# Kernel tuning notes

Hardware: AMD Instinct MI355X
Metric: run time of the kernel (lower is better)

The kernel has to match this reference:

```python
import jax, jax.numpy as jnp
import numpy as np

# Kronecker-sparse patterns (a,b,c,d), rightmost factor first, matching KSLinear.
PATTERNS = ((1, 64, 64, 64), (64, 64, 64, 1))
IN_SIZE = PATTERNS[0][0] * PATTERNS[0][2] * PATTERNS[0][3]   # 4096
OUT_SIZE = PATTERNS[-1][0] * PATTERNS[-1][1] * PATTERNS[-1][3]  # 4096
N_TOKENS = 16384


def setup_inputs() -> dict:
    key = jax.random.key(0)
    kx, k0, k1, kb = jax.random.split(key, 4)
    x = jax.random.normal(kx, (N_TOKENS, IN_SIZE), dtype=jnp.float32)
    # factors stored in native 4D (a,b,c,d) layout, uniform(-1/sqrt(c), 1/sqrt(c))
    a, b, c, d = PATTERNS[0]
    s0 = 1.0 / np.sqrt(c)
    f0 = jax.random.uniform(k0, (a, b, c, d), jnp.float32, -s0, s0)
    a, b, c, d = PATTERNS[1]
    s1 = 1.0 / np.sqrt(c)
    f1 = jax.random.uniform(k1, (a, b, c, d), jnp.float32, -s1, s1)
    bound = 1.0 / np.sqrt(IN_SIZE)
    bias = jax.random.uniform(kb, (OUT_SIZE,), jnp.float32, -bound, bound)
    return {"x": x, "f0": f0, "f1": f1, "bias": bias}


def _ks_apply(x, factor, pattern):
    # Apply one Kronecker-sparse factor with support I_a (x) 1_{b,c} (x) I_d.
    a, b, c, d = pattern
    batch = x.shape[:-1]
    x = x.reshape(*batch, a, c, d)                      # (..., a, c, d)
    y = jnp.einsum('...acd,abcd->...abd', x, factor)    # contract over c
    return y.reshape(*batch, a * b * d)


def reference(x, f0, f1, bias):
    y = _ks_apply(x, f0, PATTERNS[0])
    y = _ks_apply(y, f1, PATTERNS[1])
    return y + bias
```

## Files before the change

### kernel.cpp

```cpp
#include <hip/hip_runtime.h>
#include <cstdint>
#include <cstddef>

#define DI __device__ __forceinline__

using f32x4  = __attribute__((ext_vector_type(4))) float;
using bf16x8 = __attribute__((ext_vector_type(8))) short;
using u32x2  = __attribute__((ext_vector_type(2))) unsigned int;
using u32x4  = __attribute__((ext_vector_type(4))) unsigned int;

constexpr int NT = 16384;
constexpr int NF = 4096;

DI unsigned short f2bf(float f) {
  union { float f; unsigned u; } v; v.f = f;
  unsigned u = v.u;
  u += 0x7fffu + ((u >> 16) & 1u);
  return (unsigned short)(u >> 16);
}

DI void gload_lds16(const void* g, void* l) {
  __builtin_amdgcn_global_load_lds(
      (const __attribute__((address_space(1))) unsigned int*)g,
      (__attribute__((address_space(3))) unsigned int*)l, 16, 0, 0);
}

DI void bar_lgkm() {
  asm volatile("s_waitcnt lgkmcnt(0)" ::: "memory");
  __builtin_amdgcn_s_barrier();
  __builtin_amdgcn_sched_barrier(0);
}
#define BAR_VM(N)                                              \
  do {                                                         \
    asm volatile("s_waitcnt vmcnt(" #N ")" ::: "memory");      \
    __builtin_amdgcn_s_barrier();                              \
    __builtin_amdgcn_sched_barrier(0);                         \
  } while (0)

__global__ void ks_prep(const float* __restrict__ f0, const float* __restrict__ f1,
                        unsigned short* __restrict__ f0s, unsigned short* __restrict__ f1s) {
  int tid = blockIdx.x * 256 + threadIdx.x;
  if (tid < 262144) {
    int d = tid & 63, c = (tid >> 6) & 63, b = tid >> 12;
    f0s[d * 4096 + b * 64 + c] = f2bf(f0[tid]);
  } else {
    int t2 = tid - 262144;
    f1s[t2] = f2bf(f1[t2]);
  }
}

__global__ __launch_bounds__(512, 4) void ks1(
    const float* __restrict__ x, const unsigned short* __restrict__ f0s,
    unsigned short* __restrict__ yp)
{
  __shared__ __align__(16) char L[32768 + 2 * 16640];
  char* const Xb0 = L;
  char* const Xb1 = L + 16384;
  char* const Yb0 = L + 32768;
  char* const Yb1 = L + 32768 + 16640;

  const int w  = blockIdx.x;
  const int tt = (w & 7) | ((w >> 6) << 3);
  const int dg = (w >> 3) & 7;
  const long T0 = (long)tt * 128;

  const int tid = threadIdx.x, lane = tid & 63, wv = tid >> 6;
  const int l15 = lane & 15, lq = lane >> 4;
  const int d = dg * 8 + wv;

  bf16x8 fA[4][2];
  #pragma unroll
  for (int bt = 0; bt < 4; ++bt)
    #pragma unroll
    for (int kh = 0; kh < 2; ++kh)
      fA[bt][kh] = *(const bf16x8*)(f0s + (size_t)d * 4096 + (bt * 16 + l15) * 64 + kh * 32 + lq * 8);

  const int st_t = tid >> 5, st_c0 = (tid >> 1) & 15, st_dq = tid & 1;
  const float* const xrow0 = x + (T0 + st_t) * (long)NF + dg * 8 + st_dq * 4;
  const int wkey = (st_t & 7) << 4;

  f32x4 r0, r1, r2, r3;
  auto issue = [&](int st) {
    const float* p = xrow0 + (long)st * 16 * NF + st_c0 * 4 * 64;
    r0 = *(const f32x4*)(p);
    r1 = *(const f32x4*)(p + 64);
    r2 = *(const f32x4*)(p + 128);
    r3 = *(const f32x4*)(p + 192);
  };
  auto stageX = [&](char* X) {
    #pragma unroll
    for (int e = 0; e < 4; ++e) {
      int p = st_dq * 4 + e;
      unsigned lo = (unsigned)f2bf(r0[e]) | ((unsigned)f2bf(r1[e]) << 16);
      unsigned hi = (unsigned)f2bf(r2[e]) | ((unsigned)f2bf(r3[e]) << 16);
      *(u32x2*)(X + p * 2048 + st_t * 128 + ((st_c0 * 8) ^ wkey)) = u32x2{lo, hi};
    }
  };

  issue(0);
  stageX(Xb0);
  issue(1);
  bar_lgkm();

  const int rkey = (l15 & 7) << 4;

  for (int st = 0; st < 8; ++st) {
    char* const Xc = (st & 1) ? Xb1 : Xb0;
    char* const Xn = (st & 1) ? Xb0 : Xb1;
    char* const Yc = (st & 1) ? Yb1 : Yb0;

    const char* Xs = Xc + wv * 2048 + l15 * 128;
    bf16x8 bx0 = *(const bf16x8*)(Xs + ((0  + lq * 16) ^ rkey));
    bf16x8 bx1 = *(const bf16x8*)(Xs + ((64 + lq * 16) ^ rkey));
    f32x4 acc[4];
    #pragma unroll
    for (int bt = 0; bt < 4; ++bt) {
      acc[bt] = __builtin_amdgcn_mfma_f32_16x16x32_bf16(fA[bt][0], bx0, (f32x4){0.f,0.f,0.f,0.f}, 0, 0, 0);
      acc[bt] = __builtin_amdgcn_mfma_f32_16x16x32_bf16(fA[bt][1], bx1, acc[bt], 0, 0, 0);
    }

    {
      char* Yw = Yc + l15 * 1040 + wv * 2;
      #pragma unroll
      for (int bt = 0; bt < 4; ++bt)
        #pragma unroll
        for (int i = 0; i < 4; ++i)
          *(unsigned short*)(Yw + (bt * 16 + lq * 4 + i) * 16) = f2bf(acc[bt][i]);
    }

    stageX(Xn);
    issue(st + 2 <= 7 ? st + 2 : 7);

    bar_lgkm();

    {
      const char* Yr = Yc;
      #pragma unroll
      for (int h = 0; h < 2; ++h) {
        int t = (tid >> 6) + h * 8;
        int c16 = tid & 63;
        u32x4 v = *(const u32x4*)(Yr + t * 1040 + c16 * 16);
        *(u32x4*)(yp + (T0 + st * 16 + t) * (size_t)NF + dg * 512 + c16 * 8) = v;
      }
    }
  }
}

__global__ __launch_bounds__(512, 4) void ks2(
    const unsigned short* __restrict__ yp, const unsigned short* __restrict__ f1s,
    const float* __restrict__ bias, float* __restrict__ out)
{
  __shared__ __align__(16) char Yb[2][32768];

  const int bid = blockIdx.x;
  const int ag  = bid & 7;
  const long T0 = (long)(bid >> 3) * 256;

  const int tid = threadIdx.x, lane = tid & 63, wv = tid >> 6;
  const int l15 = lane & 15, lq = lane >> 4;
  const int a = ag * 8 + wv;

  bf16x8 fa[4][2];
  #pragma unroll
  for (int bt = 0; bt < 4; ++bt)
    #pragma unroll
    for (int kh = 0; kh < 2; ++kh)
      fa[bt][kh] = *(const bf16x8*)(f1s + (size_t)a * 4096 + (bt * 16 + l15) * 64 + kh * 32 + lq * 8);
  f32x4 bv[4];
  #pragma unroll
  for (int bt = 0; bt < 4; ++bt)
    bv[bt] = *(const f32x4*)(bias + a * 64 + bt * 16 + lq * 4);

  auto stage = [&](int tile, int buf) {
    #pragma unroll
    for (int i = 0; i < 4; ++i) {
      const int trow = i * 8 + wv;
      const int g = lane ^ (trow & 7);
      const char* src = (const char*)yp + (T0 + (long)tile * 32 + trow) * 8192
                        + ((g >> 3) << 10) + ag * 128 + (g & 7) * 16;
      gload_lds16(src, &Yb[buf][trow * 1024]);
    }
  };

  stage(0, 0);
  BAR_VM(0);

  #pragma unroll
  for (int tile = 0; tile < 8; ++tile) {
    if (tile < 7) stage(tile + 1, (tile + 1) & 1);

    const char* Yt = Yb[tile & 1];
    const int sw = wv ^ (l15 & 7);
    #pragma unroll
    for (int tt = 0; tt < 2; ++tt) {
      const char* Yr = Yt + (tt * 16 + l15) * 1024;
      bf16x8 c0 = *(const bf16x8*)(Yr + ((lq * 8 + sw) * 16));
      bf16x8 c1 = *(const bf16x8*)(Yr + (((4 + lq) * 8 + sw) * 16));
      f32x4 acc[4];
      #pragma unroll
      for (int bt = 0; bt < 4; ++bt) {
        acc[bt] = __builtin_amdgcn_mfma_f32_16x16x32_bf16(fa[bt][0], c0, (f32x4){0.f,0.f,0.f,0.f}, 0, 0, 0);
        acc[bt] = __builtin_amdgcn_mfma_f32_16x16x32_bf16(fa[bt][1], c1, acc[bt], 0, 0, 0);
      }
      float* op = out + (T0 + (long)tile * 32 + tt * 16 + l15) * NF + a * 64 + lq * 4;
      #pragma unroll
      for (int bt = 0; bt < 4; ++bt)
        *(f32x4*)(op + bt * 16) = acc[bt] + bv[bt];
    }

    BAR_VM(8);
  }
}

__global__ void ks_naive(const float* __restrict__ x, const float* __restrict__ f0,
                         const float* __restrict__ f1, const float* __restrict__ bias,
                         float* __restrict__ out)
{
  __shared__ float xr[4096];
  __shared__ float yr[4096];
  long t = blockIdx.x;
  int tid = threadIdx.x;
  for (int i = tid; i < 4096; i += 256) xr[i] = x[t * 4096 + i];
  __syncthreads();
  for (int i = tid; i < 4096; i += 256) {
    int b = i >> 6, d = i & 63;
    float s = 0.f;
    for (int c = 0; c < 64; ++c) s += xr[c * 64 + d] * f0[(b * 64 + c) * 64 + d];
    yr[i] = s;
  }
  __syncthreads();
  for (int i = tid; i < 4096; i += 256) {
    int a = i >> 6;
    float s = bias[i];
    for (int c = 0; c < 64; ++c) s += yr[a * 64 + c] * f1[(size_t)i * 64 + c];
    out[t * 4096 + i] = s;
  }
}

extern "C" void kernel_launch(void* const* d_in, const int* in_sizes, int n_in,
                              void* d_out, int out_size, void* d_ws, size_t ws_size,
                              hipStream_t stream) {
  const float* x    = (const float*)d_in[0];
  const float* f0   = (const float*)d_in[1];
  const float* f1   = (const float*)d_in[2];
  const float* bias = (const float*)d_in[3];
  float* out = (float*)d_out;

  const size_t ybytes = (size_t)NT * NF * 2;
  const size_t fbytes = (size_t)64 * 64 * 64 * 2;
  if (ws_size >= ybytes + 2 * fbytes) {
    unsigned short* yw  = (unsigned short*)d_ws;
    unsigned short* f0s = yw + (size_t)NT * NF;
    unsigned short* f1s = f0s + 64 * 64 * 64;
    ks_prep<<<2048, 256, 0, stream>>>(f0, f1, f0s, f1s);
    ks1<<<1024, 512, 0, stream>>>(x, f0s, yw);
    ks2<<<512, 512, 0, stream>>>(yw, f1s, bias, out);
  } else {
    ks_naive<<<NT, 256, 0, stream>>>(x, f0, f1, bias, out);
  }
}
```

Before: 213.0 us.

## Remap ks1 waves to (b-tile, token-half) and store Y directly from registers

Each ks1 wave now owns one 16-row b-tile for all 8 d values and a 16-token half, instead of one d value for all b-tiles. Each step stages 32 tokens, so the loop runs 4 iterations with 8 loads per thread and 128-bit LDS writes. Because each lane already holds 8 consecutive d values, results are packed and written to global memory straight from registers, which removes the Y staging buffer in LDS and its extra barrier round trip. In exchange, LDS use grows to 64 KB, the factor fragments in registers double, and occupancy may drop.

```diff
diff --git a/kernel.cpp b/kernel.cpp
--- a/kernel.cpp
+++ b/kernel.cpp
@@ -53,11 +53,9 @@
     const float* __restrict__ x, const unsigned short* __restrict__ f0s,
     unsigned short* __restrict__ yp)
 {
-  __shared__ __align__(16) char L[32768 + 2 * 16640];
+  __shared__ __align__(16) char L[65536];
   char* const Xb0 = L;
-  char* const Xb1 = L + 16384;
-  char* const Yb0 = L + 32768;
-  char* const Yb1 = L + 32768 + 16640;
+  char* const Xb1 = L + 32768;
 
   const int w  = blockIdx.x;
   const int tt = (w & 7) | ((w >> 6) << 3);
@@ -66,34 +64,34 @@
 
   const int tid = threadIdx.x, lane = tid & 63, wv = tid >> 6;
   const int l15 = lane & 15, lq = lane >> 4;
-  const int d = dg * 8 + wv;
-
-  bf16x8 fA[4][2];
-  #pragma unroll
-  for (int bt = 0; bt < 4; ++bt)
+  const int bt = wv & 3, th = wv >> 2;
+
+  bf16x8 fA[8][2];
+  #pragma unroll
+  for (int dd = 0; dd < 8; ++dd)
     #pragma unroll
     for (int kh = 0; kh < 2; ++kh)
-      fA[bt][kh] = *(const bf16x8*)(f0s + (size_t)d * 4096 + (bt * 16 + l15) * 64 + kh * 32 + lq * 8);
-
-  const int st_t = tid >> 5, st_c0 = (tid >> 1) & 15, st_dq = tid & 1;
-  const float* const xrow0 = x + (T0 + st_t) * (long)NF + dg * 8 + st_dq * 4;
+      fA[dd][kh] = *(const bf16x8*)(f0s + (size_t)(dg * 8 + dd) * 4096
+                                    + (bt * 16 + l15) * 64 + kh * 32 + lq * 8);
+
+  const int st_t = tid >> 4, st_c0 = (tid >> 1) & 7, st_dq = tid & 1;
+  const float* const xbase = x + (T0 + st_t) * (long)NF + st_c0 * 8 * 64 + dg * 8 + st_dq * 4;
   const int wkey = (st_t & 7) << 4;
 
-  f32x4 r0, r1, r2, r3;
-  auto issue = [&](int st) {
-    const float* p = xrow0 + (long)st * 16 * NF + st_c0 * 4 * 64;
-    r0 = *(const f32x4*)(p);
-    r1 = *(const f32x4*)(p + 64);
-    r2 = *(const f32x4*)(p + 128);
-    r3 = *(const f32x4*)(p + 192);
+  f32x4 v[8];
+  auto issue = [&](int k) {
+    const float* p = xbase + (long)k * 32 * NF;
+    #pragma unroll
+    for (int e = 0; e < 8; ++e) v[e] = *(const f32x4*)(p + e * 64);
   };
   auto stageX = [&](char* X) {
     #pragma unroll
-    for (int e = 0; e < 4; ++e) {
-      int p = st_dq * 4 + e;
-      unsigned lo = (unsigned)f2bf(r0[e]) | ((unsigned)f2bf(r1[e]) << 16);
-      unsigned hi = (unsigned)f2bf(r2[e]) | ((unsigned)f2bf(r3[e]) << 16);
-      *(u32x2*)(X + p * 2048 + st_t * 128 + ((st_c0 * 8) ^ wkey)) = u32x2{lo, hi};
+    for (int j = 0; j < 4; ++j) {
+      u32x4 wq;
+      #pragma unroll
+      for (int m = 0; m < 4; ++m)
+        wq[m] = (unsigned)f2bf(v[2 * m][j]) | ((unsigned)f2bf(v[2 * m + 1][j]) << 16);
+      *(u32x4*)(X + (st_dq * 4 + j) * 4096 + st_t * 128 + ((st_c0 * 16) ^ wkey)) = wq;
     }
   };
 
@@ -104,45 +102,37 @@
 
   const int rkey = (l15 & 7) << 4;
 
-  for (int st = 0; st < 8; ++st) {
-    char* const Xc = (st & 1) ? Xb1 : Xb0;
-    char* const Xn = (st & 1) ? Xb0 : Xb1;
-    char* const Yc = (st & 1) ? Yb1 : Yb0;
-
-    const char* Xs = Xc + wv * 2048 + l15 * 128;
-    bf16x8 bx0 = *(const bf16x8*)(Xs + ((0  + lq * 16) ^ rkey));
-    bf16x8 bx1 = *(const bf16x8*)(Xs + ((64 + lq * 16) ^ rkey));
-    f32x4 acc[4];
-    #pragma unroll
-    for (int bt = 0; bt < 4; ++bt) {
-      acc[bt] = __builtin_amdgcn_mfma_f32_16x16x32_bf16(fA[bt][0], bx0, (f32x4){0.f,0.f,0.f,0.f}, 0, 0, 0);
-      acc[bt] = __builtin_amdgcn_mfma_f32_16x16x32_bf16(fA[bt][1], bx1, acc[bt], 0, 0, 0);
-    }
-
-    {
-      char* Yw = Yc + l15 * 1040 + wv * 2;
-      #pragma unroll
-      for (int bt = 0; bt < 4; ++bt)
-        #pragma unroll
-        for (int i = 0; i < 4; ++i)
-          *(unsigned short*)(Yw + (bt * 16 + lq * 4 + i) * 16) = f2bf(acc[bt][i]);
-    }
-
-    stageX(Xn);
-    issue(st + 2 <= 7 ? st + 2 : 7);
+  #pragma unroll
+  for (int k = 0; k < 4; ++k) {
+    const char* const Xs = ((k & 1) ? Xb1 : Xb0) + (th * 16 + l15) * 128;
+
+    f32x4 acc[8];
+    #pragma unroll
+    for (int dd = 0; dd < 8; ++dd) {
+      const char* Xd = Xs + dd * 4096;
+      bf16x8 b0 = *(const bf16x8*)(Xd + ((lq * 16) ^ rkey));
+      bf16x8 b1 = *(const bf16x8*)(Xd + ((64 + lq * 16) ^ rkey));
+      acc[dd] = __builtin_amdgcn_mfma_f32_16x16x32_bf16(fA[dd][0], b0, (f32x4){0.f,0.f,0.f,0.f}, 0, 0, 0);
+      acc[dd] = __builtin_amdgcn_mfma_f32_16x16x32_bf16(fA[dd][1], b1, acc[dd], 0, 0, 0);
+    }
+
+    if (k < 3) {
+      stageX((k & 1) ? Xb0 : Xb1);
+      if (k < 2) issue(k + 2);
+    }
+
+    char* const yrow = (char*)yp + (T0 + k * 32 + th * 16 + l15) * 8192
+                       + dg * 1024 + (bt * 16 + lq * 4) * 16;
+    #pragma unroll
+    for (int i = 0; i < 4; ++i) {
+      u32x4 wq;
+      #pragma unroll
+      for (int m = 0; m < 4; ++m)
+        wq[m] = (unsigned)f2bf(acc[2 * m][i]) | ((unsigned)f2bf(acc[2 * m + 1][i]) << 16);
+      *(u32x4*)(yrow + i * 16) = wq;
+    }
 
     bar_lgkm();
-
-    {
-      const char* Yr = Yc;
-      #pragma unroll
-      for (int h = 0; h < 2; ++h) {
-        int t = (tid >> 6) + h * 8;
-        int c16 = tid & 63;
-        u32x4 v = *(const u32x4*)(Yr + t * 1040 + c16 * 16);
-        *(u32x4*)(yp + (T0 + st * 16 + t) * (size_t)NF + dg * 512 + c16 * 8) = v;
-      }
-    }
   }
 }
 
```

Result: slower. 261.8 us (+22.9%).
